# Kernel optimization log

Measured on AMD Instinct MI355X. Metric: run time of the kernel, lower is better.

The kernel has to match this reference:

```python
import jax, jax.numpy as jnp
import numpy as np

T, H, N, Q, C = 65536, 768, 32768, 32768, 10
MAX_LEN = 16  # max span length


def _make_spans(key, n):
    k1, k2 = jax.random.split(key)
    starts = jax.random.randint(k1, (n,), 0, T - MAX_LEN)
    lengths = jax.random.randint(k2, (n,), 1, MAX_LEN + 1)
    return jnp.stack([starts, starts + lengths], axis=1)  # [start, end)


def setup_inputs() -> dict:
    key = jax.random.key(0)
    ks = jax.random.split(key, 6)
    token_emb = jax.random.normal(ks[0], (T, H), dtype=jnp.float32)
    spans_support = _make_spans(ks[1], N)
    labels = jax.random.randint(ks[2], (N,), 0, C)
    spans_query = _make_spans(ks[3], Q)
    W_proj = jax.random.normal(ks[4], (3 * H, H), dtype=jnp.float32) * (1.0 / np.sqrt(3 * H))
    b_proj = jnp.zeros((H,), dtype=jnp.float32)
    return dict(token_emb=token_emb, spans_support=spans_support, labels=labels,
                spans_query=spans_query, W_proj=W_proj, b_proj=b_proj, n_classes=C)


def _span_embed(token_emb, spans, W, b):
    # token_emb: (T, H); spans: (n, 2) [start, end)
    s = spans[:, 0]
    e = spans[:, 1]
    # exclusive-prefix-sum trick turns per-span mean pooling into two gathers
    zero = jnp.zeros((1, token_emb.shape[1]), token_emb.dtype)
    csum = jnp.concatenate([zero, jnp.cumsum(token_emb, axis=0)], axis=0)  # (T+1, H)
    h_mean = (csum[e] - csum[s]) / (e - s).astype(token_emb.dtype)[:, None]
    feat = jnp.concatenate([token_emb[s], token_emb[e - 1], h_mean], axis=-1)  # (n, 3H)
    return jax.nn.gelu(feat @ W + b, approximate=False)  # torch nn.GELU default = erf


def _l2norm(x, eps=1e-12):
    # matches torch F.normalize: x / max(||x||, eps)
    return x / jnp.maximum(jnp.linalg.norm(x, axis=-1, keepdims=True), eps)


def reference(token_emb, spans_support, labels, spans_query, W_proj, b_proj, n_classes):
    sup = _span_embed(token_emb, spans_support, W_proj, b_proj)  # (N, H)
    qry = _span_embed(token_emb, spans_query, W_proj, b_proj)    # (Q, H)
    # prototypes = per-class mean; empty classes fall back to global mean
    sums = jax.ops.segment_sum(sup, labels, num_segments=n_classes)           # (C, H)
    counts = jax.ops.segment_sum(jnp.ones((sup.shape[0],), sup.dtype), labels,
                                 num_segments=n_classes)                       # (C,)
    gmean = sup.mean(axis=0)
    protos = jnp.where(counts[:, None] > 0,
                       sums / jnp.maximum(counts, 1.0)[:, None],
                       gmean[None, :])
    # cosine metric + constant NONE logit of 0.5
    sim = _l2norm(qry) @ _l2norm(protos).T                                     # (Q, C)
    none_logit = jnp.full((qry.shape[0], 1), 0.5, dtype=qry.dtype)
    return jnp.concatenate([sim, none_logit], axis=-1)                         # (Q, C+1)
```

## Files before the change

kernel.cpp:

```cpp
#include <hip/hip_runtime.h>
#include <stdint.h>

#define H_DIM 768
#define N_SUP 32768
#define Q_QRY 32768
#define C_CLS 10
#define M_TOT 65536
#define KG 768
#define NG 2304
#define NT 12

typedef __bf16 bf16x8 __attribute__((ext_vector_type(8)));
typedef float f32x4 __attribute__((ext_vector_type(4)));
typedef __attribute__((address_space(3))) void lds_void;
typedef const __attribute__((address_space(1))) void g_void;

__device__ __forceinline__ ushort f2bf(float f) {
  union { float f; uint32_t u; } v; v.f = f;
  uint32_t r = (v.u + 0x7FFFu + ((v.u >> 16) & 1u)) >> 16;
  return (ushort)r;
}
__device__ __forceinline__ float bf2f(ushort h) {
  union { uint32_t u; float f; } v; v.u = ((uint32_t)h) << 16; return v.f;
}
__device__ __forceinline__ float gelu_f(float x) {
  return 0.5f * x * (1.0f + erff(x * 0.70710678118654752f));
}

__global__ void cvt_kernel(const float* __restrict__ te, ushort* __restrict__ tb) {
  size_t i = (((size_t)blockIdx.x * 256) + threadIdx.x) * 8;
  float4 v0 = *(const float4*)(te + i);
  float4 v1 = *(const float4*)(te + i + 4);
  ushort4 o0, o1;
  o0.x = f2bf(v0.x); o0.y = f2bf(v0.y); o0.z = f2bf(v0.z); o0.w = f2bf(v0.w);
  o1.x = f2bf(v1.x); o1.y = f2bf(v1.y); o1.z = f2bf(v1.z); o1.w = f2bf(v1.w);
  *(ushort4*)(tb + i) = o0;
  *(ushort4*)(tb + i + 4) = o1;
}

__global__ void wt2_kernel(const float* __restrict__ W, ushort* __restrict__ Bt) {
  int idx = blockIdx.x * 256 + threadIdx.x;
  int n = idx / KG, k = idx - n * KG;
  int blk = n / H_DIM;
  int c = n - blk * H_DIM;
  Bt[idx] = f2bf(W[(size_t)(blk * H_DIM + k) * H_DIM + c]);
}

__global__ __launch_bounds__(512, 2) void gemm8(const ushort* __restrict__ A,
                                                const ushort* __restrict__ Bt,
                                                ushort* __restrict__ C) {
  __shared__ ushort lds[65536];
  char* ldsc = (char*)lds;

  int orig = blockIdx.x;
  int wg = (orig & 7) * 288 + (orig >> 3);
  int rowT = wg / 9, colT = wg - rowT * 9;
  int m0 = rowT * 256, n0 = colT * 256;

  int tid = threadIdx.x;
  int lane = tid & 63, wave = tid >> 6;
  int wr = wave >> 2, wc = wave & 3;
  int l15 = lane & 15, l4 = lane >> 4;

  int row0 = tid >> 2;
  int ss = (tid & 3) ^ ((row0 >> 1) & 3);
  size_t eA0 = (size_t)(m0 + row0) * KG + ss * 8;
  size_t eA1 = (size_t)(m0 + row0 + 128) * KG + ss * 8;
  size_t eB0 = (size_t)(n0 + row0) * KG + ss * 8;
  size_t eB1 = (size_t)(n0 + row0 + 128) * KG + ss * 8;

  int aoff[8], boff[4];
#pragma unroll
  for (int m = 0; m < 8; ++m) {
    int r = wr * 128 + m * 16 + l15;
    aoff[m] = r * 64 + ((l4 ^ ((r >> 1) & 3)) << 4);
  }
#pragma unroll
  for (int n = 0; n < 4; ++n) {
    int r = wc * 64 + n * 16 + l15;
    boff[n] = r * 64 + ((l4 ^ ((r >> 1) & 3)) << 4);
  }

  f32x4 acc[8][4];
#pragma unroll
  for (int m = 0; m < 8; ++m)
#pragma unroll
    for (int n = 0; n < 4; ++n) acc[m][n] = (f32x4){0.f, 0.f, 0.f, 0.f};

#define SLOT_A(kh, db) (ldsc + ((kh) * 2 + (db)) * 16384)
#define SLOT_B(kh, db) (ldsc + 65536 + ((kh) * 2 + (db)) * 16384)
#define STAGE_A(tk, kh, db) do { \
    char* _d = SLOT_A(kh, db) + wave * 1024; \
    size_t _k = (size_t)(tk) * 64 + (kh) * 32; \
    __builtin_amdgcn_global_load_lds((g_void*)(A + eA0 + _k), (lds_void*)_d, 16, 0, 0); \
    __builtin_amdgcn_global_load_lds((g_void*)(A + eA1 + _k), (lds_void*)(_d + 8192), 16, 0, 0); \
  } while (0)
#define STAGE_B(tk, kh, db) do { \
    char* _d = SLOT_B(kh, db) + wave * 1024; \
    size_t _k = (size_t)(tk) * 64 + (kh) * 32; \
    __builtin_amdgcn_global_load_lds((g_void*)(Bt + eB0 + _k), (lds_void*)_d, 16, 0, 0); \
    __builtin_amdgcn_global_load_lds((g_void*)(Bt + eB1 + _k), (lds_void*)(_d + 8192), 16, 0, 0); \
  } while (0)
#define LDA4(base, o) do { _Pragma("unroll") for (int m = 0; m < 4; ++m) \
    af[m] = *reinterpret_cast<const bf16x8*>((base) + aoff[(o) + m]); } while (0)
#define LDB4(base) do { _Pragma("unroll") for (int n = 0; n < 4; ++n) \
    bf[n] = *reinterpret_cast<const bf16x8*>((base) + boff[n]); } while (0)
#define MFMA_BLOCK(MB) do { _Pragma("unroll") for (int m = 0; m < 4; ++m) \
  _Pragma("unroll") for (int n = 0; n < 4; ++n) \
    acc[(MB) + m][n] = __builtin_amdgcn_mfma_f32_16x16x32_bf16(af[m], bf[n], acc[(MB) + m][n], 0, 0, 0); \
  } while (0)
#define BARX() __builtin_amdgcn_s_barrier()
#define LGKM0() asm volatile("s_waitcnt lgkmcnt(0)" ::: "memory")
#define VM8() asm volatile("s_waitcnt vmcnt(8)" ::: "memory")

  STAGE_A(0, 0, 0); STAGE_B(0, 0, 0);
  STAGE_A(0, 1, 0); STAGE_B(0, 1, 0);
  STAGE_A(1, 0, 1); STAGE_B(1, 0, 1);
  VM8();
  BARX();

  bf16x8 af[4], bf[4];
  for (int t = 0; t < NT; ++t) {
    int d = t & 1, nd = d ^ 1;
    int tk1 = (t + 1 < NT) ? t + 1 : NT - 1;
    int tk2 = (t + 2 < NT) ? t + 2 : NT - 1;
    const char* Ak0 = SLOT_A(0, d); const char* Bk0 = SLOT_B(0, d);
    const char* Ak1 = SLOT_A(1, d); const char* Bk1 = SLOT_B(1, d);
    LDA4(Ak0, 0); LDB4(Bk0);
    STAGE_A(tk1, 1, nd);
    BARX(); LGKM0();
    __builtin_amdgcn_s_setprio(1); MFMA_BLOCK(0); __builtin_amdgcn_s_setprio(0);
    BARX();
    LDA4(Ak0, 4);
    STAGE_B(tk1, 1, nd);
    BARX(); LGKM0();
    __builtin_amdgcn_s_setprio(1); MFMA_BLOCK(4); __builtin_amdgcn_s_setprio(0);
    VM8(); BARX();
    LDA4(Ak1, 0); LDB4(Bk1);
    STAGE_A(tk2, 0, d);
    BARX(); LGKM0();
    __builtin_amdgcn_s_setprio(1); MFMA_BLOCK(0); __builtin_amdgcn_s_setprio(0);
    BARX();
    LDA4(Ak1, 4);
    STAGE_B(tk2, 0, d);
    BARX(); LGKM0();
    __builtin_amdgcn_s_setprio(1); MFMA_BLOCK(4); __builtin_amdgcn_s_setprio(0);
    VM8(); BARX();
  }
  asm volatile("s_waitcnt vmcnt(0)" ::: "memory");

#pragma unroll
  for (int m = 0; m < 8; ++m)
#pragma unroll
    for (int n = 0; n < 4; ++n) {
      int col = n0 + wc * 64 + n * 16 + l15;
      size_t rb = (size_t)(m0 + wr * 128 + m * 16 + l4 * 4) * NG + col;
#pragma unroll
      for (int v = 0; v < 4; ++v)
        C[rb + (size_t)v * NG] = f2bf(acc[m][n][v]);
    }
#undef SLOT_A
#undef SLOT_B
#undef STAGE_A
#undef STAGE_B
#undef LDA4
#undef LDB4
#undef MFMA_BLOCK
}

__global__ void combine_kernel(const ushort* __restrict__ PQR, const int* __restrict__ spS,
                               const int* __restrict__ spQ, const float* __restrict__ bias,
                               ushort* __restrict__ emb) {
  int wid = (int)((((size_t)blockIdx.x * blockDim.x) + threadIdx.x) >> 6);
  int lane = threadIdx.x & 63;
  if (wid >= M_TOT) return;
  int s, e;
  if (wid < N_SUP) { s = spS[2 * wid]; e = spS[2 * wid + 1]; }
  else             { int w = wid - N_SUP; s = spQ[2 * w]; e = spQ[2 * w + 1]; }
  int len = e - s;
  float inv = 1.0f / (float)len;

  float acc0[3][4], accr[3][4];
  const ushort* Pr = PQR + (size_t)s * NG;
  const ushort* Qr = PQR + (size_t)(e - 1) * NG + 768;
#pragma unroll
  for (int c = 0; c < 3; ++c) {
    int h = c * 256 + lane * 4;
    ushort4 p = *(const ushort4*)(Pr + h);
    ushort4 q = *(const ushort4*)(Qr + h);
    acc0[c][0] = bf2f(p.x) + bf2f(q.x);
    acc0[c][1] = bf2f(p.y) + bf2f(q.y);
    acc0[c][2] = bf2f(p.z) + bf2f(q.z);
    acc0[c][3] = bf2f(p.w) + bf2f(q.w);
    accr[c][0] = accr[c][1] = accr[c][2] = accr[c][3] = 0.f;
  }
  for (int r = s; r < e; ++r) {
    const ushort* Rr = PQR + (size_t)r * NG + 1536;
#pragma unroll
    for (int c = 0; c < 3; ++c) {
      int h = c * 256 + lane * 4;
      ushort4 rv = *(const ushort4*)(Rr + h);
      accr[c][0] += bf2f(rv.x); accr[c][1] += bf2f(rv.y);
      accr[c][2] += bf2f(rv.z); accr[c][3] += bf2f(rv.w);
    }
  }
  ushort* er = emb + (size_t)wid * H_DIM;
#pragma unroll
  for (int c = 0; c < 3; ++c) {
    int h = c * 256 + lane * 4;
    float4 bv = *(const float4*)(bias + h);
    ushort4 o;
    o.x = f2bf(gelu_f(acc0[c][0] + accr[c][0] * inv + bv.x));
    o.y = f2bf(gelu_f(acc0[c][1] + accr[c][1] * inv + bv.y));
    o.z = f2bf(gelu_f(acc0[c][2] + accr[c][2] * inv + bv.z));
    o.w = f2bf(gelu_f(acc0[c][3] + accr[c][3] * inv + bv.w));
    *(ushort4*)(er + h) = o;
  }
}

__global__ void proto_accum(const ushort* __restrict__ supEmb, const int* __restrict__ labels,
                            float* __restrict__ pSum, float* __restrict__ pCnt) {
  __shared__ float ls[C_CLS * H_DIM];
  __shared__ int lc[C_CLS];
  int t = threadIdx.x;
  for (int i = t; i < C_CLS * H_DIM; i += 256) ls[i] = 0.f;
  if (t < C_CLS) lc[t] = 0;
  __syncthreads();
  int base = blockIdx.x * 128;
  for (int si = 0; si < 128; ++si) {
    int sp = base + si;
    int lab = labels[sp];
    const ushort* er = supEmb + (size_t)sp * H_DIM;
#pragma unroll
    for (int j = 0; j < 3; ++j) {
      int c = t + j * 256;
      ls[lab * H_DIM + c] += bf2f(er[c]);
    }
    if (t == 0) lc[lab]++;
  }
  __syncthreads();
  for (int i = t; i < C_CLS * H_DIM; i += 256) atomicAdd(&pSum[i], ls[i]);
  if (t < C_CLS) atomicAdd(&pCnt[t], (float)lc[t]);
}

__global__ void proto_norm(const float* __restrict__ pSum, const float* __restrict__ pCnt,
                           float* __restrict__ pN) {
  __shared__ float red[4];
  int t = threadIdx.x, lane = t & 63, wave = t >> 6;
  for (int c = 0; c < C_CLS; ++c) {
    float cnt = pCnt[c];
    float x[3];
#pragma unroll
    for (int j = 0; j < 3; ++j) {
      int h = t + j * 256;
      float v;
      if (cnt > 0.5f) v = pSum[c * H_DIM + h] / cnt;
      else {
        float gs = 0.f;
        for (int cc = 0; cc < C_CLS; ++cc) gs += pSum[cc * H_DIM + h];
        v = gs / (float)N_SUP;
      }
      x[j] = v;
    }
    float ss = x[0] * x[0] + x[1] * x[1] + x[2] * x[2];
#pragma unroll
    for (int o = 32; o; o >>= 1) ss += __shfl_xor(ss, o);
    if (lane == 0) red[wave] = ss;
    __syncthreads();
    float tot = red[0] + red[1] + red[2] + red[3];
    float inv = 1.0f / fmaxf(sqrtf(tot), 1e-12f);
#pragma unroll
    for (int j = 0; j < 3; ++j) pN[c * H_DIM + t + j * 256] = x[j] * inv;
    __syncthreads();
  }
}

__global__ void sim_kernel(const ushort* __restrict__ emb, const float* __restrict__ pN,
                           float* __restrict__ out) {
  __shared__ float lp[C_CLS * H_DIM];
  int t = threadIdx.x;
  for (int i = t; i < C_CLS * H_DIM; i += 256) lp[i] = pN[i];
  __syncthreads();
  int lane = t & 63, wave = t >> 6;
  for (int row = blockIdx.x * 4 + wave; row < Q_QRY; row += gridDim.x * 4) {
    const ushort* qr = emb + (size_t)(N_SUP + row) * H_DIM;
    float dot[C_CLS] = {0, 0, 0, 0, 0, 0, 0, 0, 0, 0};
    float sq = 0.f;
#pragma unroll
    for (int j = 0; j < 12; ++j) {
      float v = bf2f(qr[lane + 64 * j]);
      sq += v * v;
#pragma unroll
      for (int p = 0; p < C_CLS; ++p) dot[p] += v * lp[p * H_DIM + lane + 64 * j];
    }
#pragma unroll
    for (int o = 32; o; o >>= 1) {
      sq += __shfl_xor(sq, o);
#pragma unroll
      for (int p = 0; p < C_CLS; ++p) dot[p] += __shfl_xor(dot[p], o);
    }
    if (lane == 0) {
      float inv = 1.0f / fmaxf(sqrtf(sq), 1e-12f);
      float* o = out + (size_t)row * (C_CLS + 1);
      o[0] = dot[0] * inv; o[1] = dot[1] * inv; o[2] = dot[2] * inv;
      o[3] = dot[3] * inv; o[4] = dot[4] * inv; o[5] = dot[5] * inv;
      o[6] = dot[6] * inv; o[7] = dot[7] * inv; o[8] = dot[8] * inv;
      o[9] = dot[9] * inv; o[10] = 0.5f;
    }
  }
}

extern "C" void kernel_launch(void* const* d_in, const int* in_sizes, int n_in,
                              void* d_out, int out_size, void* d_ws, size_t ws_size,
                              hipStream_t stream) {
  const float* token_emb = (const float*)d_in[0];
  const int*   spansS    = (const int*)d_in[1];
  const int*   labels    = (const int*)d_in[2];
  const int*   spansQ    = (const int*)d_in[3];
  const float* W         = (const float*)d_in[4];
  const float* b         = (const float*)d_in[5];
  float* out = (float*)d_out;

  char* ws = (char*)d_ws;
  size_t pqrB = (size_t)M_TOT * NG * 2;
  size_t embB = (size_t)M_TOT * H_DIM * 2;
  size_t wtB  = (size_t)NG * KG * 2;
  ushort* PQR  = (ushort*)ws;
  ushort* tebf = (ushort*)(ws + pqrB);
  ushort* emb  = tebf;
  ushort* Bt   = (ushort*)(ws + pqrB + embB);
  float*  pSum = (float*)(ws + pqrB + embB + wtB);
  float*  pCnt = pSum + C_CLS * H_DIM;
  float*  pN   = pCnt + 64;

  hipMemsetAsync(pSum, 0, (C_CLS * H_DIM + 64) * sizeof(float), stream);
  cvt_kernel<<<24576, 256, 0, stream>>>(token_emb, tebf);
  wt2_kernel<<<6912, 256, 0, stream>>>(W, Bt);
  gemm8<<<2304, 512, 0, stream>>>(tebf, Bt, PQR);
  combine_kernel<<<16384, 256, 0, stream>>>(PQR, spansS, spansQ, b, emb);
  proto_accum<<<N_SUP / 128, 256, 0, stream>>>(emb, labels, pSum, pCnt);
  proto_norm<<<1, 256, 0, stream>>>(pSum, pCnt, pN);
  sim_kernel<<<512, 256, 0, stream>>>(emb, pN, out);
}
```

Measured before the change: 630.1 us.

## Bucket-sort spans by start token to improve PQR gather locality in combine

Adds a histogram, prefix-scan and scatter pass that sorts all spans into buckets of 64 tokens by start position. The combine kernel then walks spans in sorted order, with an XCD-aware block swizzle, so waves that share a block or XCD touch nearby rows of the large PQR matrix and get better L2/MALL reuse. The bf16 conversion and weight transpose kernels are merged into one prep launch that also builds the histogram. This adds two small serial launches and atomics in exchange for more local gathers in combine.

```diff
diff --git a/kernel.cpp b/kernel.cpp
--- a/kernel.cpp
+++ b/kernel.cpp
@@ -9,6 +9,7 @@
 #define KG 768
 #define NG 2304
 #define NT 12
+#define NBUCK 1024
 
 typedef __bf16 bf16x8 __attribute__((ext_vector_type(8)));
 typedef float f32x4 __attribute__((ext_vector_type(4)));
@@ -27,23 +28,65 @@
   return 0.5f * x * (1.0f + erff(x * 0.70710678118654752f));
 }
 
-__global__ void cvt_kernel(const float* __restrict__ te, ushort* __restrict__ tb) {
-  size_t i = (((size_t)blockIdx.x * 256) + threadIdx.x) * 8;
-  float4 v0 = *(const float4*)(te + i);
-  float4 v1 = *(const float4*)(te + i + 4);
-  ushort4 o0, o1;
-  o0.x = f2bf(v0.x); o0.y = f2bf(v0.y); o0.z = f2bf(v0.z); o0.w = f2bf(v0.w);
-  o1.x = f2bf(v1.x); o1.y = f2bf(v1.y); o1.z = f2bf(v1.z); o1.w = f2bf(v1.w);
-  *(ushort4*)(tb + i) = o0;
-  *(ushort4*)(tb + i + 4) = o1;
-}
-
-__global__ void wt2_kernel(const float* __restrict__ W, ushort* __restrict__ Bt) {
-  int idx = blockIdx.x * 256 + threadIdx.x;
-  int n = idx / KG, k = idx - n * KG;
-  int blk = n / H_DIM;
-  int c = n - blk * H_DIM;
-  Bt[idx] = f2bf(W[(size_t)(blk * H_DIM + k) * H_DIM + c]);
+__global__ void prep_kernel(const float* __restrict__ te, const float* __restrict__ W,
+                            const int* __restrict__ spS, const int* __restrict__ spQ,
+                            ushort* __restrict__ tb, ushort* __restrict__ Bt,
+                            int* __restrict__ hist) {
+  int b = blockIdx.x, t = threadIdx.x;
+  if (b < 24576) {
+    size_t i = (((size_t)b * 256) + t) * 8;
+    float4 v0 = *(const float4*)(te + i);
+    float4 v1 = *(const float4*)(te + i + 4);
+    ushort4 o0, o1;
+    o0.x = f2bf(v0.x); o0.y = f2bf(v0.y); o0.z = f2bf(v0.z); o0.w = f2bf(v0.w);
+    o1.x = f2bf(v1.x); o1.y = f2bf(v1.y); o1.z = f2bf(v1.z); o1.w = f2bf(v1.w);
+    *(ushort4*)(tb + i) = o0;
+    *(ushort4*)(tb + i + 4) = o1;
+  } else if (b < 31488) {
+    int idx = (b - 24576) * 256 + t;
+    int n = idx / KG, k = idx - n * KG;
+    int blk = n / H_DIM;
+    int c = n - blk * H_DIM;
+    Bt[idx] = f2bf(W[(size_t)(blk * H_DIM + k) * H_DIM + c]);
+  } else {
+    __shared__ int lh[NBUCK];
+    for (int i = t; i < NBUCK; i += 256) lh[i] = 0;
+    __syncthreads();
+    int b0 = b - 31488;
+    for (int i = b0 * 256 + t; i < M_TOT; i += 64 * 256) {
+      int s = (i < N_SUP) ? spS[2 * i] : spQ[2 * (i - N_SUP)];
+      atomicAdd(&lh[s >> 6], 1);
+    }
+    __syncthreads();
+    for (int i = t; i < NBUCK; i += 256) if (lh[i]) atomicAdd(&hist[i], lh[i]);
+  }
+}
+
+__global__ void prefix_kernel(const int* __restrict__ hist, int* __restrict__ cursor) {
+  __shared__ int tmp[NBUCK];
+  int t = threadIdx.x;
+  int v = hist[t];
+  tmp[t] = v;
+  __syncthreads();
+  for (int off = 1; off < NBUCK; off <<= 1) {
+    int add = (t >= off) ? tmp[t - off] : 0;
+    __syncthreads();
+    tmp[t] += add;
+    __syncthreads();
+  }
+  cursor[t] = tmp[t] - v;
+}
+
+__global__ void scatter_kernel(const int* __restrict__ spS, const int* __restrict__ spQ,
+                               int* __restrict__ cursor, int2* __restrict__ sorted) {
+  for (int i = blockIdx.x * 256 + threadIdx.x; i < M_TOT; i += gridDim.x * 256) {
+    int s, e;
+    if (i < N_SUP) { s = spS[2 * i]; e = spS[2 * i + 1]; }
+    else           { int w = i - N_SUP; s = spQ[2 * w]; e = spQ[2 * w + 1]; }
+    int pos = atomicAdd(&cursor[s >> 6], 1);
+    int2 rec; rec.x = s; rec.y = (i << 5) | (e - s);
+    sorted[pos] = rec;
+  }
 }
 
 __global__ __launch_bounds__(512, 2) void gemm8(const ushort* __restrict__ A,
@@ -168,16 +211,19 @@
 #undef MFMA_BLOCK
 }
 
-__global__ void combine_kernel(const ushort* __restrict__ PQR, const int* __restrict__ spS,
-                               const int* __restrict__ spQ, const float* __restrict__ bias,
-                               ushort* __restrict__ emb) {
-  int wid = (int)((((size_t)blockIdx.x * blockDim.x) + threadIdx.x) >> 6);
-  int lane = threadIdx.x & 63;
-  if (wid >= M_TOT) return;
-  int s, e;
-  if (wid < N_SUP) { s = spS[2 * wid]; e = spS[2 * wid + 1]; }
-  else             { int w = wid - N_SUP; s = spQ[2 * w]; e = spQ[2 * w + 1]; }
-  int len = e - s;
+__global__ __launch_bounds__(256) void combine2(const ushort* __restrict__ PQR,
+                                                const int2* __restrict__ sorted,
+                                                const float* __restrict__ bias,
+                                                ushort* __restrict__ emb) {
+  int b = blockIdx.x;
+  int sb = ((b & 7) << 11) + (b >> 3);
+  int wave = threadIdx.x >> 6, lane = threadIdx.x & 63;
+  int wid = sb * 4 + wave;
+  int2 rec = sorted[wid];
+  int s = rec.x;
+  int len = rec.y & 31;
+  int orig = rec.y >> 5;
+  int e = s + len;
   float inv = 1.0f / (float)len;
 
   float acc0[3][4], accr[3][4];
@@ -204,7 +250,7 @@
       accr[c][2] += bf2f(rv.z); accr[c][3] += bf2f(rv.w);
     }
   }
-  ushort* er = emb + (size_t)wid * H_DIM;
+  ushort* er = emb + (size_t)orig * H_DIM;
 #pragma unroll
   for (int c = 0; c < 3; ++c) {
     int h = c * 256 + lane * 4;
@@ -329,15 +375,21 @@
   ushort* tebf = (ushort*)(ws + pqrB);
   ushort* emb  = tebf;
   ushort* Bt   = (ushort*)(ws + pqrB + embB);
-  float*  pSum = (float*)(ws + pqrB + embB + wtB);
+  char*   tail = ws + pqrB + embB + wtB;
+  float*  pSum = (float*)tail;
   float*  pCnt = pSum + C_CLS * H_DIM;
   float*  pN   = pCnt + 64;
+  int*    hist = (int*)(pN + C_CLS * H_DIM);
+  int*    cursor = hist + NBUCK;
+  int2*   sorted = (int2*)(cursor + NBUCK);
 
   hipMemsetAsync(pSum, 0, (C_CLS * H_DIM + 64) * sizeof(float), stream);
-  cvt_kernel<<<24576, 256, 0, stream>>>(token_emb, tebf);
-  wt2_kernel<<<6912, 256, 0, stream>>>(W, Bt);
+  hipMemsetAsync(hist, 0, NBUCK * sizeof(int), stream);
+  prep_kernel<<<31552, 256, 0, stream>>>(token_emb, W, spansS, spansQ, tebf, Bt, hist);
+  prefix_kernel<<<1, NBUCK, 0, stream>>>(hist, cursor);
+  scatter_kernel<<<64, 256, 0, stream>>>(spansS, spansQ, cursor, sorted);
   gemm8<<<2304, 512, 0, stream>>>(tebf, Bt, PQR);
-  combine_kernel<<<16384, 256, 0, stream>>>(PQR, spansS, spansQ, b, emb);
+  combine2<<<16384, 256, 0, stream>>>(PQR, sorted, b, emb);
   proto_accum<<<N_SUP / 128, 256, 0, stream>>>(emb, labels, pSum, pCnt);
   proto_norm<<<1, 256, 0, stream>>>(pSum, pCnt, pN);
   sim_kernel<<<512, 256, 0, stream>>>(emb, pN, out);
```

After: 598.9 us. 1.05x faster.
